# Performance work log

Measured on AMD Instinct MI355X. Metric: run time of the kernel, lower is better.

Reference implementation:

```python
import jax, jax.numpy as jnp
import numpy as np

BETA = 0.25
N_EMBED = 16384
EMBED_DIM = 256

def setup_inputs() -> dict:
    key = jax.random.key(0)
    k1, k2 = jax.random.split(key)
    z = jax.random.normal(k1, (16, 256, 32, 32), dtype=jnp.float32)
    # codebook initialized uniform(-1/n_embed, 1/n_embed) as in the torch module
    W = jax.random.uniform(k2, (N_EMBED, EMBED_DIM), dtype=jnp.float32,
                           minval=-1.0 / N_EMBED, maxval=1.0 / N_EMBED)
    return {"z": z, "W": W}

def reference(z, W):
    # z: [B, C, H, W] with C == embed_dim; W: [n_embed, embed_dim]
    zt = jnp.transpose(z, (0, 2, 3, 1))            # [B, H, W, C]
    zf = zt.reshape(-1, W.shape[1])                # [N, C], N = B*H*W
    # squared euclidean distances: ||z||^2 + ||e||^2 - 2 z.e
    d = (jnp.sum(zf * zf, axis=1, keepdims=True)
         + jnp.sum(W * W, axis=1)
         - 2.0 * jnp.einsum('nd,kd->nk', zf, W))   # [N, n_embed]
    idx = jnp.argmin(d, axis=1)                    # [N] int32
    z_q = W[idx].reshape(zt.shape)                 # [B, H, W, C]
    sg = jax.lax.stop_gradient
    loss = (BETA * jnp.mean((sg(z_q) - zt) ** 2)
            + jnp.mean((z_q - sg(zt)) ** 2))
    z_q = zt + sg(z_q - zt)                        # straight-through
    z_q = jnp.transpose(z_q, (0, 3, 1, 2))         # back to [B, C, H, W]
    return (z_q, loss, idx)
```

## Files before the change

### kernel.cpp

```cpp
#include <hip/hip_runtime.h>
#include <cstdint>


using u64 = unsigned long long;
using u32 = unsigned int;

#define NVEC   16384
#define NEMB   16384
#define DEPTH  256
#define LOSS_OFF 4194304
#define IDX_OFF  4194305
#define CAPD  5.0e-4f
#define ENCD  (255.0f/CAPD)
#define DECD  (CAPD/255.0f)

typedef __bf16 bf16x8 __attribute__((ext_vector_type(8)));
typedef float  f32x4  __attribute__((ext_vector_type(4)));

__device__ __forceinline__ void gld16(const void* g, void* l) {
    __builtin_amdgcn_global_load_lds(
        (const __attribute__((address_space(1))) char*)g,
        (__attribute__((address_space(3))) char*)l, 16, 0, 0);
}
__device__ __forceinline__ u64 umin64(u64 a, u64 b) { return a < b ? a : b; }
__device__ __forceinline__ u64 umax64(u64 a, u64 b) { return a > b ? a : b; }
__device__ __forceinline__ u64 pk7(float m, u32 k) { return ((u64)__float_as_uint(m) << 7) | k; }
__device__ __forceinline__ float upk7(u64 key) { return __uint_as_float((u32)(key >> 7)); }
__device__ __forceinline__ u32 q8(float d) {
    int v = (int)fminf(d * ENCD, 255.0f) - 1;
    return (u32)(v < 0 ? 0 : v);
}

__global__ __launch_bounds__(256) void k_prep_w(const float* __restrict__ W,
                                                __bf16* __restrict__ Wh,
                                                float* __restrict__ wnorm2,
                                                float* __restrict__ out) {
    if (blockIdx.x == 0 && threadIdx.x == 0) out[LOSS_OFF] = 0.0f;
    int t = threadIdx.x, w = t >> 6, lane = t & 63;
    int row = blockIdx.x * 4 + w;
    const float4 v = *reinterpret_cast<const float4*>(W + (size_t)row * DEPTH + lane * 4);
    __bf16 h0 = (__bf16)v.x, h1 = (__bf16)v.y, h2 = (__bf16)v.z, h3 = (__bf16)v.w;
    ushort4 pk;
    pk.x = __builtin_bit_cast(unsigned short, h0);
    pk.y = __builtin_bit_cast(unsigned short, h1);
    pk.z = __builtin_bit_cast(unsigned short, h2);
    pk.w = __builtin_bit_cast(unsigned short, h3);
    *reinterpret_cast<ushort4*>(Wh + (size_t)row * DEPTH + lane * 4) = pk;
    float n2 = v.x * v.x + v.y * v.y + v.z * v.z + v.w * v.w;
#pragma unroll
    for (int s = 32; s > 0; s >>= 1) n2 += __shfl_down(n2, s, 64);
    if (lane == 0) wnorm2[row] = n2;
}

__global__ __launch_bounds__(256) void k_wmax(const float* __restrict__ wnorm2,
                                              u32* __restrict__ wmax2) {
    __shared__ float red[256];
    int t = threadIdx.x;
    float m = 0.0f;
    for (int i = t; i < NEMB; i += 256) m = fmaxf(m, wnorm2[i]);
    red[t] = m;
    __syncthreads();
    for (int s = 128; s > 0; s >>= 1) {
        if (t < s) red[t] = fmaxf(red[t], red[t + s]);
        __syncthreads();
    }
    if (t == 0) *wmax2 = __float_as_uint(red[0]);
}

__global__ __launch_bounds__(256) void k_prep_z(const float* __restrict__ z, __bf16* __restrict__ Zh) {
    __shared__ float tile[64][65];
    int hw0 = blockIdx.x * 64, c0 = blockIdx.y * 64, b = blockIdx.z;
    int t = threadIdx.x, lane = t & 63, grp = t >> 6;
    const float* zb = z + (size_t)b * 262144;
    for (int cc = grp; cc < 64; cc += 4)
        tile[cc][lane] = zb[(size_t)(c0 + cc) * 1024 + hw0 + lane];
    __syncthreads();
    for (int hh = grp; hh < 64; hh += 4)
        Zh[(size_t)(b * 1024 + hw0 + hh) * DEPTH + c0 + lane] = (__bf16)tile[lane][hh];
}

__global__ __launch_bounds__(256) void k_rownorm(const float* __restrict__ z, float* __restrict__ sz) {
    __shared__ float red[4][64];
    int bid = blockIdx.x;
    int b = bid >> 4, hw0 = (bid & 15) << 6;
    int t = threadIdx.x, r = t & 63, cg = t >> 6;
    const float* zp = z + b * 262144 + hw0 + r;
    float acc = 0.0f;
    for (int c = cg; c < DEPTH; c += 4) {
        float v = zp[c * 1024];
        acc = fmaf(v, v, acc);
    }
    red[cg][r] = acc;
    __syncthreads();
    if (t < 64)
        sz[bid * 64 + t] = (red[0][t] + red[1][t]) + (red[2][t] + red[3][t]);
}

__global__ __launch_bounds__(256) void k_transpose_w(const float* __restrict__ W, float* __restrict__ Wt) {
    __shared__ float tile[64][65];
    int k0 = blockIdx.x * 64;
    int d0 = blockIdx.y * 64;
    int t = threadIdx.x, lane = t & 63, grp = t >> 6;
    for (int kk = grp; kk < 64; kk += 4)
        tile[kk][lane] = W[(k0 + kk) * DEPTH + d0 + lane];
    __syncthreads();
    for (int dd = grp; dd < 64; dd += 4)
        Wt[(size_t)(d0 + dd) * NEMB + k0 + lane] = tile[lane][dd];
}

__global__ __launch_bounds__(256, 4) void k_gemm(const __bf16* __restrict__ Wh,
                                                 const __bf16* __restrict__ Zh,
                                                 const float* __restrict__ sz,
                                                 u64* __restrict__ tilePack) {
    __shared__ __bf16 As[128 * 64];
    __shared__ __bf16 Bs[128 * 64];
    const int kt = blockIdx.x, nt = blockIdx.y;
    const int k0 = kt * 128, n0 = nt * 128;
    const int t = threadIdx.x, w = t >> 6, lane = t & 63;
    const int quad = lane >> 4, l15 = lane & 15;
    const int wy = w >> 1, wx = w & 1;

    const int rowS = w * 8 + (lane >> 3);
    const int colb = (((lane & 7) ^ (lane >> 3)) * 8);
    const __bf16* gA = Wh + (size_t)(k0 + rowS) * DEPTH + colb;
    const __bf16* gB = Zh + (size_t)(n0 + rowS) * DEPTH + colb;
    __bf16* lA = As + w * 8 * 64;
    __bf16* lB = Bs + w * 8 * 64;

    f32x4 acc[4][4] = {};
    float szq[4];
#pragma unroll
    for (int fj = 0; fj < 4; ++fj)
        szq[fj] = sz[n0 + wx * 64 + fj * 16 + l15];

    for (int kb = 0; kb < 4; ++kb) {
        __syncthreads();
#pragma unroll
        for (int j = 0; j < 4; ++j) {
            gld16(gA + kb * 64 + j * 32 * DEPTH, lA + j * 32 * 64);
            gld16(gB + kb * 64 + j * 32 * DEPTH, lB + j * 32 * 64);
        }
        __syncthreads();
#pragma unroll
        for (int ks = 0; ks < 2; ++ks) {
            const int ph = ((ks * 4 + quad) ^ (l15 & 7)) * 8;
            bf16x8 a[4], b[4];
#pragma unroll
            for (int fi = 0; fi < 4; ++fi)
                a[fi] = *reinterpret_cast<const bf16x8*>(As + (wy * 64 + fi * 16 + l15) * 64 + ph);
#pragma unroll
            for (int fj = 0; fj < 4; ++fj)
                b[fj] = *reinterpret_cast<const bf16x8*>(Bs + (wx * 64 + fj * 16 + l15) * 64 + ph);
#pragma unroll
            for (int fi = 0; fi < 4; ++fi)
#pragma unroll
                for (int fj = 0; fj < 4; ++fj)
                    acc[fi][fj] = __builtin_amdgcn_mfma_f32_16x16x32_bf16(a[fi], b[fj], acc[fi][fj], 0, 0, 0);
        }
    }

    __syncthreads();
    float* s_m1 = reinterpret_cast<float*>(As);
    float* s_m2 = s_m1 + 256;
    float* s_m3 = s_m2 + 256;
    u32*   s_k1 = reinterpret_cast<u32*>(s_m3 + 256);
    u32*   s_k2 = s_k1 + 256;

#pragma unroll
    for (int fj = 0; fj < 4; ++fj) {
#pragma unroll
        for (int fi = 0; fi < 4; ++fi)
#pragma unroll
            for (int r = 0; r < 4; ++r)
                acc[fi][fj][r] = fmaf(-2.0f, acc[fi][fj][r], szq[fj]);
        float m1 = 3.4e38f, m2 = 3.4e38f, m3 = 3.4e38f;
#pragma unroll
        for (int fi = 0; fi < 4; ++fi)
#pragma unroll
            for (int r = 0; r < 4; ++r) {
                float x = acc[fi][fj][r];
                float t1 = fmaxf(m1, x); m1 = fminf(m1, x);
                float t2 = fmaxf(m2, t1); m2 = fminf(m2, t1);
                m3 = fminf(m3, t2);
            }
#pragma unroll
        for (int mm = 16; mm <= 32; mm <<= 1) {
            float o1 = __shfl_xor(m1, mm, 64);
            float o2 = __shfl_xor(m2, mm, 64);
            float o3 = __shfl_xor(m3, mm, 64);
            float c1 = fminf(m1, o1), x1 = fmaxf(m1, o1);
            float c2 = fminf(m2, o2), x2 = fmaxf(m2, o2);
            float n2 = fminf(x1, c2);
            float n3 = fminf(fminf(m3, o3), fminf(fmaxf(x1, c2), x2));
            m1 = c1; m2 = n2; m3 = n3;
        }
        u32 kl = 0xFFFFu;
#pragma unroll
        for (int fi = 3; fi >= 0; --fi)
#pragma unroll
            for (int r = 3; r >= 0; --r) {
                float x = acc[fi][fj][r];
                u32 cd = (u32)(wy * 64 + fi * 16 + quad * 4 + r);
                kl = (x == m1) ? cd : kl;
            }
#pragma unroll
        for (int mm = 16; mm <= 32; mm <<= 1) {
            u32 ok = __shfl_xor(kl, mm, 64);
            kl = kl < ok ? kl : ok;
        }
        u32 kl2 = 0xFFFFu;
#pragma unroll
        for (int fi = 3; fi >= 0; --fi)
#pragma unroll
            for (int r = 3; r >= 0; --r) {
                float x = acc[fi][fj][r];
                u32 cd = (u32)(wy * 64 + fi * 16 + quad * 4 + r);
                kl2 = (x == m2 && cd != kl) ? cd : kl2;
            }
#pragma unroll
        for (int mm = 16; mm <= 32; mm <<= 1) {
            u32 ok = __shfl_xor(kl2, mm, 64);
            kl2 = kl2 < ok ? kl2 : ok;
        }
        if (quad == 0) {
            int q = wx * 64 + fj * 16 + l15;
            s_m1[q * 2 + wy] = m1; s_m2[q * 2 + wy] = m2; s_m3[q * 2 + wy] = m3;
            s_k1[q * 2 + wy] = kl; s_k2[q * 2 + wy] = kl2;
        }
    }
    __syncthreads();
    if (t < 128) {
        int n = n0 + t;
        u64 A1 = pk7(s_m1[t * 2 + 0], s_k1[t * 2 + 0]);
        u64 A2 = pk7(s_m2[t * 2 + 0], s_k2[t * 2 + 0]);
        u64 B1 = pk7(s_m1[t * 2 + 1], s_k1[t * 2 + 1]);
        u64 B2 = pk7(s_m2[t * 2 + 1], s_k2[t * 2 + 1]);
        u64 c1 = umin64(A1, B1), x1 = umax64(A1, B1);
        u64 c2 = umin64(A2, B2), X2 = umax64(A2, B2);
        u64 s2 = umin64(x1, c2);
        float f3 = fminf(fminf(s_m3[t * 2], s_m3[t * 2 + 1]),
                         fminf(upk7(umax64(x1, c2)), upk7(X2)));
        float M1 = upk7(c1); u32 K1 = (u32)(c1 & 0x7F);
        float M2 = upk7(s2); u32 K2 = (u32)(s2 & 0x7F);
        u32 d2q = q8(M2 - M1);
        u32 d3q = q8(f3 - M1);
        u32 lo = (d2q << 24) | (d3q << 16) | (K1 << 9) | (K2 << 2);
        tilePack[(size_t)kt * NVEC + n] = ((u64)__float_as_uint(M1) << 32) | lo;
    }
}

__global__ __launch_bounds__(256) void k_refine(const float* __restrict__ z,
                                                const float* __restrict__ W,
                                                const float* __restrict__ Wt,
                                                const float* __restrict__ sz,
                                                const u32* __restrict__ wmax2,
                                                const u64* __restrict__ tp,
                                                u64* __restrict__ best) {
    __shared__ float zt[16][264];
    __shared__ u32 hi[128][17];
    __shared__ u32 lo[128][17];
    __shared__ u32 qn[16][64];
    __shared__ u64 qk[16][25];
    __shared__ u32 ccnt[16], tcnt[16], ovf[16];
    __shared__ u32 tlist[128];
    __shared__ u32 tnum;
    const int n0 = blockIdx.x * 16;
    const int b = n0 >> 10, hw0 = n0 & 1023;
    const int t = threadIdx.x;

    if (t < 16) { ccnt[t] = 0u; tcnt[t] = 0u; ovf[t] = 0u; }
    if (t == 16) tnum = 0u;
    for (int i = t; i < 16 * 25; i += 256) (&qk[0][0])[i] = ~0ull;
    {
        int r = t & 15, ktg = t >> 4;
#pragma unroll
        for (int p = 0; p < 8; ++p) {
            int kt = p * 16 + ktg;
            u64 v = tp[(size_t)kt * NVEC + n0 + r];
            hi[kt][r] = (u32)(v >> 32);
            lo[kt][r] = (u32)v;
        }
    }
    {
        int hw = t & 15, cg = t >> 4;
        const float* zb = z + (size_t)b * 262144 + hw0 + hw;
#pragma unroll
        for (int i = 0; i < 16; ++i) {
            int c = i * 16 + cg;
            zt[hw][c] = zb[(size_t)c * 1024];
        }
    }
    __syncthreads();

    const float wmaxv = sqrtf(__uint_as_float(*wmax2));
    const int w = t >> 6, lane = t & 63;

    for (int rr = w; rr < 16; rr += 4) {
        const int n = n0 + rr;
        float f0 = __uint_as_float(hi[lane][rr]);
        float f1 = __uint_as_float(hi[lane + 64][rr]);
        float g = fminf(f0, f1);
#pragma unroll
        for (int mm = 1; mm < 64; mm <<= 1) g = fminf(g, __shfl_xor(g, mm, 64));
        const float E = 0.008f * sqrtf(sz[n]) * wmaxv + 5.0e-5f;
        const float tau = g + 2.0f * E;
#pragma unroll
        for (int half = 0; half < 2; ++half) {
            int kt = lane + half * 64;
            float m1 = half ? f1 : f0;
            if (m1 <= tau) {
                u32 lw = lo[kt][rr];
                u32 p = atomicAdd(&ccnt[rr], 1u);
                if (p < 64u) qn[rr][p] = (u32)kt * 128u + ((lw >> 9) & 0x7Fu);
                else ovf[rr] = 1u;
                float rem = tau - m1;
                float d2 = (float)((lw >> 24) & 0xFFu) * DECD;
                if (d2 <= rem) {
                    u32 p2 = atomicAdd(&ccnt[rr], 1u);
                    if (p2 < 64u) qn[rr][p2] = (u32)kt * 128u + ((lw >> 2) & 0x7Fu);
                    else ovf[rr] = 1u;
                }
                float d3 = (float)((lw >> 16) & 0xFFu) * DECD;
                if (d3 <= rem) {
                    u32 j = atomicAdd(&tcnt[rr], 1u);
                    if (j < 8u) {
                        u32 gi = atomicAdd(&tnum, 1u);
                        tlist[gi] = ((u32)rr << 10) | (j << 7) | (u32)kt;
                    } else ovf[rr] = 1u;
                }
            }
        }
    }
    __syncthreads();

    {
        int rr = t >> 4, slot0 = t & 15;
        u32 cn = ccnt[rr]; if (cn > 64u) cn = 64u;
        u64 mykey = ~0ull;
        bool any = false;
#pragma unroll
        for (int sgi = 0; sgi < 4; ++sgi) {
            u32 slot = (u32)slot0 + (u32)sgi * 16u;
            if (slot < cn) {
                u32 kg = qn[rr][slot];
                const float4* wr = reinterpret_cast<const float4*>(W + (size_t)kg * DEPTH);
                const float4* zv4 = reinterpret_cast<const float4*>(&zt[rr][0]);
                float a = 0.0f;
                for (int c = 0; c < 64; ++c) {
                    float4 wv = wr[c]; float4 zv = zv4[c];
                    a = fmaf(zv.x, wv.x, a); a = fmaf(zv.y, wv.y, a);
                    a = fmaf(zv.z, wv.z, a); a = fmaf(zv.w, wv.w, a);
                }
                float dv = sz[n0 + rr] - 2.0f * a;
                mykey = umin64(mykey, ((u64)__float_as_uint(dv) << 32) | kg);
                any = true;
            }
        }
        if (any) qk[rr][slot0] = mykey;
    }
    {
        u32 tn = tnum;
        for (u32 i = (u32)w; i < tn; i += 4) {
            u32 e = tlist[i];
            int rr = e >> 10, j = (e >> 7) & 7, kt = e & 0x7F;
            u32 k_a = (u32)kt * 128u + (u32)lane, k_b = k_a + 64u;
            const float* zr = &zt[rr][0];
            float a0 = 0.0f, a1 = 0.0f;
            for (int c = 0; c < DEPTH; ++c) {
                float zc = zr[c];
                const float* wc = Wt + (size_t)c * NEMB + (u32)kt * 128u;
                a0 = fmaf(zc, wc[lane], a0);
                a1 = fmaf(zc, wc[lane + 64], a1);
            }
            float szv = sz[n0 + rr];
            u64 key = umin64(((u64)__float_as_uint(szv - 2.0f * a0) << 32) | k_a,
                             ((u64)__float_as_uint(szv - 2.0f * a1) << 32) | k_b);
#pragma unroll
            for (int mm = 1; mm < 64; mm <<= 1)
                key = umin64(key, __shfl_xor(key, mm, 64));
            if (lane == 0) qk[rr][16 + j] = key;
        }
    }
    for (int rr = w; rr < 16; rr += 4) {
        if (ovf[rr]) {
            const float* zr = &zt[rr][0];
            float szv = sz[n0 + rr];
            u64 mk = ~0ull;
            for (int kg = lane; kg < NEMB; kg += 64) {
                float a = 0.0f;
                for (int c = 0; c < DEPTH; ++c)
                    a = fmaf(zr[c], Wt[(size_t)c * NEMB + kg], a);
                mk = umin64(mk, ((u64)__float_as_uint(szv - 2.0f * a) << 32) | (u32)kg);
            }
#pragma unroll
            for (int mm = 1; mm < 64; mm <<= 1)
                mk = umin64(mk, __shfl_xor(mk, mm, 64));
            if (lane == 0) qk[rr][24] = mk;
        }
    }
    __syncthreads();
    if (t < 16) {
        u64 m = qk[t][0];
#pragma unroll
        for (int j = 1; j < 25; ++j) m = umin64(m, qk[t][j]);
        best[n0 + t] = m;
    }
}

__global__ __launch_bounds__(256) void k_epilogue(const float* __restrict__ z,
                                                  const float* __restrict__ Wc,
                                                  const u64* __restrict__ best,
                                                  float* __restrict__ out,
                                                  float* __restrict__ lossacc) {
    __shared__ unsigned kk[64];
    __shared__ float red[256];
    int bid = blockIdx.x;
    int b = bid >> 4, hw0 = (bid & 15) << 6;
    int n0 = bid << 6;
    int t = threadIdx.x, r = t & 63, cg = t >> 6;
    if (t < 64) {
        unsigned ki = (unsigned)(best[n0 + t] & 0xffffffffull) & 0x3FFFu;
        kk[t] = ki;
        out[IDX_OFF + n0 + t] = (float)ki;
    }
    __syncthreads();
    const float* wrow = Wc + (size_t)kk[r] * DEPTH;
    int zbase = b * 262144 + hw0 + r;
    float part = 0.0f;
    for (int c = cg; c < DEPTH; c += 4) {
        float wv = wrow[c];
        float zv = z[zbase + c * 1024];
        out[zbase + c * 1024] = wv;
        float df = wv - zv;
        part = fmaf(df, df, part);
    }
    red[t] = part;
    __syncthreads();
    for (int s = 128; s > 0; s >>= 1) {
        if (t < s) red[t] += red[t + s];
        __syncthreads();
    }
    if (t == 0) atomicAdd(lossacc, red[0]);
}

__global__ void k_loss_final(float* __restrict__ out) {
    out[LOSS_OFF] = out[LOSS_OFF] * (1.25f / 4194304.0f);
}

extern "C" void kernel_launch(void* const* d_in, const int* in_sizes, int n_in,
                              void* d_out, int out_size, void* d_ws, size_t ws_size,
                              hipStream_t stream) {
    const float* z = (const float*)d_in[0];
    const float* W = (const float*)d_in[1];
    float* out = (float*)d_out;
    char* ws = (char*)d_ws;

    __bf16* Zh    = (__bf16*)ws;
    __bf16* Wh    = (__bf16*)(ws + 8388608);
    float*  Wt    = (float*)ws;
    float*  sz    = (float*) (ws + 16777216);
    u64*    best  = (u64*)   (ws + 16842752);
    u32*    wmax2 = (u32*)   (ws + 16973824);

    float* wnorm2   = out;
    u64*   tilePack = (u64*)out;
    float* lossacc  = out + LOSS_OFF;

    k_prep_w     <<<dim3(4096),      dim3(256), 0, stream>>>(W, Wh, wnorm2, out);
    k_wmax       <<<dim3(1),         dim3(256), 0, stream>>>(wnorm2, wmax2);
    k_prep_z     <<<dim3(16, 4, 16), dim3(256), 0, stream>>>(z, Zh);
    k_rownorm    <<<dim3(256),       dim3(256), 0, stream>>>(z, sz);
    k_gemm       <<<dim3(128, 128),  dim3(256), 0, stream>>>(Wh, Zh, sz, tilePack);
    k_transpose_w<<<dim3(256, 4),    dim3(256), 0, stream>>>(W, Wt);
    k_refine     <<<dim3(1024),      dim3(256), 0, stream>>>(z, W, Wt, sz, wmax2, tilePack, best);
    k_epilogue   <<<dim3(256),       dim3(256), 0, stream>>>(z, W, best, out, lossacc);
    k_loss_final <<<dim3(1),         dim3(1),   0, stream>>>(out);
}
```

Measured before the change: 379.7 us.

## Double-buffer GEMM LDS loads and fuse prep kernels into one launch

Merges the W conversion, z transpose-to-bf16 and z row-norm kernels into one launch that branches on block index. The wmax reduction becomes a 16-block atomicMax, and the loss scaling moves into the epilogue atomic so the final one-thread kernel is dropped. The GEMM main loop changes from 4 steps of 64 columns with two barriers each to 8 double-buffered steps of 32 columns, prefetching the next slice while MFMAs run, with a new swizzle. This cuts launch overhead and exposed load latency, at the cost of more loop iterations and a reliance on async-load ordering with one barrier per step.

```diff
diff --git a/kernel.cpp b/kernel.cpp
--- a/kernel.cpp
+++ b/kernel.cpp
@@ -31,69 +31,77 @@
     return (u32)(v < 0 ? 0 : v);
 }
 
-__global__ __launch_bounds__(256) void k_prep_w(const float* __restrict__ W,
-                                                __bf16* __restrict__ Wh,
-                                                float* __restrict__ wnorm2,
-                                                float* __restrict__ out) {
-    if (blockIdx.x == 0 && threadIdx.x == 0) out[LOSS_OFF] = 0.0f;
-    int t = threadIdx.x, w = t >> 6, lane = t & 63;
-    int row = blockIdx.x * 4 + w;
-    const float4 v = *reinterpret_cast<const float4*>(W + (size_t)row * DEPTH + lane * 4);
-    __bf16 h0 = (__bf16)v.x, h1 = (__bf16)v.y, h2 = (__bf16)v.z, h3 = (__bf16)v.w;
-    ushort4 pk;
-    pk.x = __builtin_bit_cast(unsigned short, h0);
-    pk.y = __builtin_bit_cast(unsigned short, h1);
-    pk.z = __builtin_bit_cast(unsigned short, h2);
-    pk.w = __builtin_bit_cast(unsigned short, h3);
-    *reinterpret_cast<ushort4*>(Wh + (size_t)row * DEPTH + lane * 4) = pk;
-    float n2 = v.x * v.x + v.y * v.y + v.z * v.z + v.w * v.w;
-#pragma unroll
-    for (int s = 32; s > 0; s >>= 1) n2 += __shfl_down(n2, s, 64);
-    if (lane == 0) wnorm2[row] = n2;
+__global__ __launch_bounds__(256) void k_front(const float* __restrict__ W,
+                                               __bf16* __restrict__ Wh,
+                                               float* __restrict__ wnorm2,
+                                               float* __restrict__ out,
+                                               const float* __restrict__ z,
+                                               __bf16* __restrict__ Zh,
+                                               float* __restrict__ sz,
+                                               u32* __restrict__ wmax2) {
+    __shared__ float tile[64][65];
+    __shared__ float red[4][64];
+    const int bid = blockIdx.x;
+    const int t = threadIdx.x;
+    if (bid < 4096) {
+        if (bid == 0 && t == 0) { out[LOSS_OFF] = 0.0f; *wmax2 = 0u; }
+        int w = t >> 6, lane = t & 63;
+        int row = bid * 4 + w;
+        const float4 v = *reinterpret_cast<const float4*>(W + (size_t)row * DEPTH + lane * 4);
+        __bf16 h0 = (__bf16)v.x, h1 = (__bf16)v.y, h2 = (__bf16)v.z, h3 = (__bf16)v.w;
+        ushort4 pk;
+        pk.x = __builtin_bit_cast(unsigned short, h0);
+        pk.y = __builtin_bit_cast(unsigned short, h1);
+        pk.z = __builtin_bit_cast(unsigned short, h2);
+        pk.w = __builtin_bit_cast(unsigned short, h3);
+        *reinterpret_cast<ushort4*>(Wh + (size_t)row * DEPTH + lane * 4) = pk;
+        float n2 = v.x * v.x + v.y * v.y + v.z * v.z + v.w * v.w;
+#pragma unroll
+        for (int s = 32; s > 0; s >>= 1) n2 += __shfl_down(n2, s, 64);
+        if (lane == 0) wnorm2[row] = n2;
+    } else if (bid < 5120) {
+        int b2 = bid - 4096;
+        int hw0 = (b2 & 15) * 64, c0 = ((b2 >> 4) & 3) * 64, b = b2 >> 6;
+        int lane = t & 63, grp = t >> 6;
+        const float* zb = z + (size_t)b * 262144;
+        for (int cc = grp; cc < 64; cc += 4)
+            tile[cc][lane] = zb[(size_t)(c0 + cc) * 1024 + hw0 + lane];
+        __syncthreads();
+        for (int hh = grp; hh < 64; hh += 4)
+            Zh[(size_t)(b * 1024 + hw0 + hh) * DEPTH + c0 + lane] = (__bf16)tile[lane][hh];
+    } else {
+        int b3 = bid - 5120;
+        int b = b3 >> 4, hw0 = (b3 & 15) << 6;
+        int r = t & 63, cg = t >> 6;
+        const float* zp = z + b * 262144 + hw0 + r;
+        float acc = 0.0f;
+        for (int c = cg; c < DEPTH; c += 4) {
+            float v = zp[c * 1024];
+            acc = fmaf(v, v, acc);
+        }
+        red[cg][r] = acc;
+        __syncthreads();
+        if (t < 64)
+            sz[b3 * 64 + t] = (red[0][t] + red[1][t]) + (red[2][t] + red[3][t]);
+    }
 }
 
 __global__ __launch_bounds__(256) void k_wmax(const float* __restrict__ wnorm2,
                                               u32* __restrict__ wmax2) {
-    __shared__ float red[256];
+    __shared__ float red4[4];
     int t = threadIdx.x;
+    int base = blockIdx.x * 1024 + t;
     float m = 0.0f;
-    for (int i = t; i < NEMB; i += 256) m = fmaxf(m, wnorm2[i]);
-    red[t] = m;
-    __syncthreads();
-    for (int s = 128; s > 0; s >>= 1) {
-        if (t < s) red[t] = fmaxf(red[t], red[t + s]);
-        __syncthreads();
-    }
-    if (t == 0) *wmax2 = __float_as_uint(red[0]);
-}
-
-__global__ __launch_bounds__(256) void k_prep_z(const float* __restrict__ z, __bf16* __restrict__ Zh) {
-    __shared__ float tile[64][65];
-    int hw0 = blockIdx.x * 64, c0 = blockIdx.y * 64, b = blockIdx.z;
-    int t = threadIdx.x, lane = t & 63, grp = t >> 6;
-    const float* zb = z + (size_t)b * 262144;
-    for (int cc = grp; cc < 64; cc += 4)
-        tile[cc][lane] = zb[(size_t)(c0 + cc) * 1024 + hw0 + lane];
-    __syncthreads();
-    for (int hh = grp; hh < 64; hh += 4)
-        Zh[(size_t)(b * 1024 + hw0 + hh) * DEPTH + c0 + lane] = (__bf16)tile[lane][hh];
-}
-
-__global__ __launch_bounds__(256) void k_rownorm(const float* __restrict__ z, float* __restrict__ sz) {
-    __shared__ float red[4][64];
-    int bid = blockIdx.x;
-    int b = bid >> 4, hw0 = (bid & 15) << 6;
-    int t = threadIdx.x, r = t & 63, cg = t >> 6;
-    const float* zp = z + b * 262144 + hw0 + r;
-    float acc = 0.0f;
-    for (int c = cg; c < DEPTH; c += 4) {
-        float v = zp[c * 1024];
-        acc = fmaf(v, v, acc);
-    }
-    red[cg][r] = acc;
-    __syncthreads();
-    if (t < 64)
-        sz[bid * 64 + t] = (red[0][t] + red[1][t]) + (red[2][t] + red[3][t]);
+#pragma unroll
+    for (int j = 0; j < 4; ++j) m = fmaxf(m, wnorm2[base + j * 256]);
+#pragma unroll
+    for (int s = 32; s > 0; s >>= 1) m = fmaxf(m, __shfl_down(m, s, 64));
+    if ((t & 63) == 0) red4[t >> 6] = m;
+    __syncthreads();
+    if (t == 0) {
+        m = fmaxf(fmaxf(red4[0], red4[1]), fmaxf(red4[2], red4[3]));
+        atomicMax(wmax2, __float_as_uint(m));
+    }
 }
 
 __global__ __launch_bounds__(256) void k_transpose_w(const float* __restrict__ W, float* __restrict__ Wt) {
@@ -112,20 +120,24 @@
                                                  const __bf16* __restrict__ Zh,
                                                  const float* __restrict__ sz,
                                                  u64* __restrict__ tilePack) {
-    __shared__ __bf16 As[128 * 64];
-    __shared__ __bf16 Bs[128 * 64];
+    __shared__ __align__(16) __bf16 As[2][128 * 32];
+    __shared__ __align__(16) __bf16 Bs[2][128 * 32];
     const int kt = blockIdx.x, nt = blockIdx.y;
     const int k0 = kt * 128, n0 = nt * 128;
     const int t = threadIdx.x, w = t >> 6, lane = t & 63;
     const int quad = lane >> 4, l15 = lane & 15;
     const int wy = w >> 1, wx = w & 1;
 
-    const int rowS = w * 8 + (lane >> 3);
-    const int colb = (((lane & 7) ^ (lane >> 3)) * 8);
-    const __bf16* gA = Wh + (size_t)(k0 + rowS) * DEPTH + colb;
-    const __bf16* gB = Zh + (size_t)(n0 + rowS) * DEPTH + colb;
-    __bf16* lA = As + w * 8 * 64;
-    __bf16* lB = Bs + w * 8 * 64;
+    const int srow = lane >> 2;
+    const int schunk = (lane & 3) ^ (srow & 3);
+    const __bf16* gA = Wh + (size_t)(k0 + w * 32 + srow) * DEPTH + schunk * 8;
+    const __bf16* gB = Zh + (size_t)(n0 + w * 32 + srow) * DEPTH + schunk * 8;
+
+#pragma unroll
+    for (int h = 0; h < 2; ++h) {
+        gld16(gA + h * 16 * DEPTH, &As[0][(w * 32 + h * 16) * 32]);
+        gld16(gB + h * 16 * DEPTH, &Bs[0][(w * 32 + h * 16) * 32]);
+    }
 
     f32x4 acc[4][4] = {};
     float szq[4];
@@ -133,34 +145,36 @@
     for (int fj = 0; fj < 4; ++fj)
         szq[fj] = sz[n0 + wx * 64 + fj * 16 + l15];
 
-    for (int kb = 0; kb < 4; ++kb) {
+    const int rdsw = (quad ^ (l15 & 3)) * 8;
+    __syncthreads();
+
+#pragma unroll
+    for (int kb = 0; kb < 8; ++kb) {
+        const int p = kb & 1;
+        if (kb < 7) {
+            const int q = p ^ 1;
+#pragma unroll
+            for (int h = 0; h < 2; ++h) {
+                gld16(gA + (kb + 1) * 32 + h * 16 * DEPTH, &As[q][(w * 32 + h * 16) * 32]);
+                gld16(gB + (kb + 1) * 32 + h * 16 * DEPTH, &Bs[q][(w * 32 + h * 16) * 32]);
+            }
+        }
+        bf16x8 a[4], b[4];
+#pragma unroll
+        for (int fi = 0; fi < 4; ++fi)
+            a[fi] = *reinterpret_cast<const bf16x8*>(&As[p][(wy * 64 + fi * 16 + l15) * 32 + rdsw]);
+#pragma unroll
+        for (int fj = 0; fj < 4; ++fj)
+            b[fj] = *reinterpret_cast<const bf16x8*>(&Bs[p][(wx * 64 + fj * 16 + l15) * 32 + rdsw]);
+#pragma unroll
+        for (int fi = 0; fi < 4; ++fi)
+#pragma unroll
+            for (int fj = 0; fj < 4; ++fj)
+                acc[fi][fj] = __builtin_amdgcn_mfma_f32_16x16x32_bf16(a[fi], b[fj], acc[fi][fj], 0, 0, 0);
         __syncthreads();
-#pragma unroll
-        for (int j = 0; j < 4; ++j) {
-            gld16(gA + kb * 64 + j * 32 * DEPTH, lA + j * 32 * 64);
-            gld16(gB + kb * 64 + j * 32 * DEPTH, lB + j * 32 * 64);
-        }
-        __syncthreads();
-#pragma unroll
-        for (int ks = 0; ks < 2; ++ks) {
-            const int ph = ((ks * 4 + quad) ^ (l15 & 7)) * 8;
-            bf16x8 a[4], b[4];
-#pragma unroll
-            for (int fi = 0; fi < 4; ++fi)
-                a[fi] = *reinterpret_cast<const bf16x8*>(As + (wy * 64 + fi * 16 + l15) * 64 + ph);
-#pragma unroll
-            for (int fj = 0; fj < 4; ++fj)
-                b[fj] = *reinterpret_cast<const bf16x8*>(Bs + (wx * 64 + fj * 16 + l15) * 64 + ph);
-#pragma unroll
-            for (int fi = 0; fi < 4; ++fi)
-#pragma unroll
-                for (int fj = 0; fj < 4; ++fj)
-                    acc[fi][fj] = __builtin_amdgcn_mfma_f32_16x16x32_bf16(a[fi], b[fj], acc[fi][fj], 0, 0, 0);
-        }
-    }
-
-    __syncthreads();
-    float* s_m1 = reinterpret_cast<float*>(As);
+    }
+
+    float* s_m1 = reinterpret_cast<float*>(&As[0][0]);
     float* s_m2 = s_m1 + 256;
     float* s_m3 = s_m2 + 256;
     u32*   s_k1 = reinterpret_cast<u32*>(s_m3 + 256);
@@ -440,11 +454,7 @@
         if (t < s) red[t] += red[t + s];
         __syncthreads();
     }
-    if (t == 0) atomicAdd(lossacc, red[0]);
-}
-
-__global__ void k_loss_final(float* __restrict__ out) {
-    out[LOSS_OFF] = out[LOSS_OFF] * (1.25f / 4194304.0f);
+    if (t == 0) atomicAdd(lossacc, red[0] * (1.25f / 4194304.0f));
 }
 
 extern "C" void kernel_launch(void* const* d_in, const int* in_sizes, int n_in,
@@ -466,13 +476,10 @@
     u64*   tilePack = (u64*)out;
     float* lossacc  = out + LOSS_OFF;
 
-    k_prep_w     <<<dim3(4096),      dim3(256), 0, stream>>>(W, Wh, wnorm2, out);
-    k_wmax       <<<dim3(1),         dim3(256), 0, stream>>>(wnorm2, wmax2);
-    k_prep_z     <<<dim3(16, 4, 16), dim3(256), 0, stream>>>(z, Zh);
-    k_rownorm    <<<dim3(256),       dim3(256), 0, stream>>>(z, sz);
-    k_gemm       <<<dim3(128, 128),  dim3(256), 0, stream>>>(Wh, Zh, sz, tilePack);
-    k_transpose_w<<<dim3(256, 4),    dim3(256), 0, stream>>>(W, Wt);
-    k_refine     <<<dim3(1024),      dim3(256), 0, stream>>>(z, W, Wt, sz, wmax2, tilePack, best);
-    k_epilogue   <<<dim3(256),       dim3(256), 0, stream>>>(z, W, best, out, lossacc);
-    k_loss_final <<<dim3(1),         dim3(1),   0, stream>>>(out);
-}
+    k_front      <<<dim3(5376),     dim3(256), 0, stream>>>(W, Wh, wnorm2, out, z, Zh, sz, wmax2);
+    k_wmax       <<<dim3(16),       dim3(256), 0, stream>>>(wnorm2, wmax2);
+    k_gemm       <<<dim3(128, 128), dim3(256), 0, stream>>>(Wh, Zh, sz, tilePack);
+    k_transpose_w<<<dim3(256, 4),   dim3(256), 0, stream>>>(W, Wt);
+    k_refine     <<<dim3(1024),     dim3(256), 0, stream>>>(z, W, Wt, sz, wmax2, tilePack, best);
+    k_epilogue   <<<dim3(256),      dim3(256), 0, stream>>>(z, W, best, out, lossacc);
+}
```

Result: faster. 355.6 us (-6.4%).
